# Kernel optimization log

Measured on AMD Instinct MI355X. Metric: run time of the kernel, lower is better.

Reference implementation:

```python
import jax, jax.numpy as jnp
import numpy as np

D_MODEL = 1024
D_K = 64
D_V = 64
TEMPERATURE = float(np.sqrt(D_K))
LN_EPS = 1e-5


def setup_inputs() -> dict:
    key = jax.random.key(0)
    ks = jax.random.split(key, 8)
    B, L = 8, 2048
    q = jax.random.normal(ks[0], (B, L, D_K), dtype=jnp.float32)
    k = jax.random.normal(ks[1], (B, L, D_K), dtype=jnp.float32)
    v = jax.random.normal(ks[2], (B, L, D_V), dtype=jnp.float32)
    residual = jax.random.normal(ks[3], (B, L, D_MODEL), dtype=jnp.float32)
    # fc: Linear(d_v, d_model), xavier-normal weight, zero-ish bias
    fc_w = jax.random.normal(ks[4], (D_MODEL, D_V), dtype=jnp.float32) * float(np.sqrt(2.0 / (D_V + D_MODEL)))
    fc_b = jnp.zeros((D_MODEL,), dtype=jnp.float32)
    ln_gamma = jnp.ones((D_MODEL,), dtype=jnp.float32)
    ln_beta = jnp.zeros((D_MODEL,), dtype=jnp.float32)
    return {"q": q, "k": k, "v": v, "residual": residual,
            "fc_w": fc_w, "fc_b": fc_b, "ln_gamma": ln_gamma, "ln_beta": ln_beta}


def reference(q, k, v, residual, fc_w, fc_b, ln_gamma, ln_beta):
    # scaled dot-product attention: scores [B, Lq, Lk]
    scores = jnp.einsum("bqd,bkd->bqk", q, k) / TEMPERATURE
    # module computes both log_softmax and softmax (shared logsumexp in a
    # fused kernel); log_attn is discarded by Attention.forward
    log_attn = jax.nn.log_softmax(scores, axis=2)
    attn = jnp.exp(log_attn)  # == softmax(scores); dropout is identity at eval
    out = jnp.einsum("bqk,bkv->bqv", attn, v)  # [B, Lq, d_v]
    # fc + residual + LayerNorm (dropout identity at eval)
    out = jnp.einsum("bqv,mv->bqm", out, fc_w) + fc_b
    x = out + residual
    mu = jnp.mean(x, axis=-1, keepdims=True)
    var = jnp.var(x, axis=-1, keepdims=True)
    return (x - mu) * jax.lax.rsqrt(var + LN_EPS) * ln_gamma + ln_beta
```

## Files before the change

### kernel.cpp

```cpp
#include <hip/hip_runtime.h>

typedef float  f32x4 __attribute__((ext_vector_type(4)));
typedef float  f4v   __attribute__((ext_vector_type(4)));
typedef short  s16x8 __attribute__((ext_vector_type(8)));
typedef unsigned short u16x4 __attribute__((ext_vector_type(4)));
typedef unsigned short u16;

#define DEVI static __device__ __forceinline__
#define AS1 __attribute__((address_space(1)))
#define AS3 __attribute__((address_space(3)))

DEVI u16 f2bf(float f) {
  unsigned int u = __builtin_bit_cast(unsigned int, f);
  u += 0x7FFFu + ((u >> 16) & 1u);
  return (u16)(u >> 16);
}

constexpr int B  = 8;
constexpr int L  = 2048;
constexpr int D  = 64;
constexpr int DM = 1024;

__global__ void prep_kernel(const float* __restrict__ k, const float* __restrict__ v,
                            const float* __restrict__ w,
                            u16* __restrict__ kbf, u16* __restrict__ vtbf,
                            u16* __restrict__ wbf) {
  __shared__ float tile[64 * 65];
  const int bid = blockIdx.x, tid = threadIdx.x;
  if (bid < 1024) {
    const int i = bid * 256 + tid;
    f4v f = ((const f4v*)k)[i];
    u16x4 o;
#pragma unroll
    for (int j = 0; j < 4; ++j) o[j] = f2bf(f[j] * 0.125f);
    ((u16x4*)kbf)[i] = o;
  } else if (bid < 1024 + 64) {
    const int i = (bid - 1024) * 256 + tid;
    f4v f = ((const f4v*)w)[i];
    u16x4 o;
#pragma unroll
    for (int j = 0; j < 4; ++j) o[j] = f2bf(f[j]);
    ((u16x4*)wbf)[i] = o;
  } else {
    const int t2 = bid - 1088;
    const int b = t2 >> 5, tt = t2 & 31;
    const float* vp = v + ((size_t)b * L + tt * 64) * D;
    for (int i = tid; i < 4096; i += 256) {
      const int r = i >> 6, c = i & 63;
      tile[c * 65 + r] = vp[i];
    }
    __syncthreads();
    u16* op = vtbf + (size_t)b * D * L + tt * 64;
    for (int i = tid; i < 4096; i += 256) {
      const int dv = i >> 6, kv = i & 63;
      op[(size_t)dv * L + kv] = f2bf(tile[dv * 65 + kv]);
    }
  }
}

__global__ __launch_bounds__(512) void attn_kernel(const float* __restrict__ q,
                                                   const u16* __restrict__ kbf,
                                                   const u16* __restrict__ vtbf,
                                                   float* __restrict__ Og) {
  const int blk = blockIdx.x;
  const int b = blk >> 5;
  const int qrow0 = (blk & 31) * 64;
  const int tid = threadIdx.x;
  const int wave = tid >> 6, lane = tid & 63;
  const int g = wave >> 1, h = wave & 1;
  const int lg = lane >> 4, ln = lane & 15;

  __shared__ __align__(16) u16   Kt[2][64 * 64];
  __shared__ __align__(16) u16   Vt[2][64 * 64];
  __shared__ __align__(16) u16   Pl[8][16 * 40];
  __shared__ float Macc[8][16][68];
  __shared__ float Lsum[8][16];

  s16x8 aq[2];
  {
    const float* qp = q + ((size_t)b * L + qrow0 + g * 16 + ln) * D + lg * 8;
#pragma unroll
    for (int kk = 0; kk < 2; ++kk) {
      f4v f0 = *(const f4v*)(qp + kk * 32);
      f4v f1 = *(const f4v*)(qp + kk * 32 + 4);
      s16x8 a;
#pragma unroll
      for (int j = 0; j < 4; ++j) { a[j] = (short)f2bf(f0[j]); a[4 + j] = (short)f2bf(f1[j]); }
      aq[kk] = a;
    }
  }

  const f32x4 zf = {0.f, 0.f, 0.f, 0.f};
  f32x4 acc[4];
#pragma unroll
  for (int i = 0; i < 4; ++i) acc[i] = zf;
  float lrow[4] = {0.f, 0.f, 0.f, 0.f};

  const u16* kb = kbf + (size_t)b * L * D;
  const u16* vb = vtbf + (size_t)b * D * L;

  auto stage = [&](int buf, int t) {
    const int kv0 = t * 64;
    const int row = tid >> 3, jl = tid & 7;
    const int js = jl ^ (row & 7);
    const u16* srcK = kb + (size_t)(kv0 + row) * D + js * 8;
    __builtin_amdgcn_global_load_lds(
        (const AS1 unsigned int*)srcK, (AS3 unsigned int*)&Kt[buf][tid * 8], 16, 0, 0);
    const u16* srcV = vb + (size_t)row * L + kv0 + js * 8;
    __builtin_amdgcn_global_load_lds(
        (const AS1 unsigned int*)srcV, (AS3 unsigned int*)&Vt[buf][tid * 8], 16, 0, 0);
  };

  stage(0, 0);

  for (int t = 0; t < 32; ++t) {
    __syncthreads();
    if (t + 1 < 32) stage((t + 1) & 1, t + 1);
    const int buf = t & 1;

    f32x4 s[2];
    s[0] = zf; s[1] = zf;
#pragma unroll
    for (int kk = 0; kk < 2; ++kk) {
#pragma unroll
      for (int fn2 = 0; fn2 < 2; ++fn2) {
        const int kvr = h * 32 + fn2 * 16 + ln;
        const int j = (kk * 4 + lg) ^ (kvr & 7);
        s16x8 bk = *(const s16x8*)&Kt[buf][kvr * 64 + j * 8];
        s[fn2] = __builtin_amdgcn_mfma_f32_16x16x32_bf16(aq[kk], bk, s[fn2], 0, 0, 0);
      }
    }

#pragma unroll
    for (int r = 0; r < 4; ++r) {
      const float p0 = __expf(s[0][r]);
      const float p1 = __expf(s[1][r]);
      lrow[r] += p0 + p1;
      Pl[wave][(lg * 4 + r) * 40 + ln]      = f2bf(p0);
      Pl[wave][(lg * 4 + r) * 40 + 16 + ln] = f2bf(p1);
    }

    asm volatile("" ::: "memory");

    s16x8 ap = *(const s16x8*)&Pl[wave][ln * 40 + lg * 8];
#pragma unroll
    for (int fn = 0; fn < 4; ++fn) {
      const int dv = fn * 16 + ln;
      const int j = (h * 4 + lg) ^ (dv & 7);
      s16x8 bv = *(const s16x8*)&Vt[buf][dv * 64 + j * 8];
      acc[fn] = __builtin_amdgcn_mfma_f32_16x16x32_bf16(ap, bv, acc[fn], 0, 0, 0);
    }
  }

#pragma unroll
  for (int r = 0; r < 4; ++r) {
#pragma unroll
    for (int off = 1; off < 16; off <<= 1) lrow[r] += __shfl_xor(lrow[r], off, 64);
    if (ln == 0) Lsum[wave][lg * 4 + r] = lrow[r];
  }
#pragma unroll
  for (int fn = 0; fn < 4; ++fn)
#pragma unroll
    for (int r = 0; r < 4; ++r)
      Macc[wave][lg * 4 + r][fn * 16 + ln] = acc[fn][r];
  __syncthreads();

  {
    const int row = tid >> 3, d0 = (tid & 7) * 8;
    const int g2 = row >> 4, r2 = row & 15;
    const float linv = 1.f / (Lsum[g2 * 2][r2] + Lsum[g2 * 2 + 1][r2]);
    f4v o0 = *(const f4v*)&Macc[g2 * 2][r2][d0]     + *(const f4v*)&Macc[g2 * 2 + 1][r2][d0];
    f4v o1 = *(const f4v*)&Macc[g2 * 2][r2][d0 + 4] + *(const f4v*)&Macc[g2 * 2 + 1][r2][d0 + 4];
#pragma unroll
    for (int j = 0; j < 4; ++j) { o0[j] *= linv; o1[j] *= linv; }
    float* dst = Og + ((size_t)b * L + qrow0 + row) * D + d0;
    *(f4v*)dst = o0;
    *(f4v*)(dst + 4) = o1;
  }
}

__global__ __launch_bounds__(512, 2) void fc_ln_kernel(const float* __restrict__ Og,
                                                       const u16* __restrict__ wbf,
                                                       const float* __restrict__ bias,
                                                       const float* __restrict__ resid,
                                                       const float* __restrict__ gamma,
                                                       const float* __restrict__ beta,
                                                       float* __restrict__ out) {
  __shared__ __align__(16) u16   Wl[1024 * 64];
  __shared__ __align__(16) float bl[1024];
  __shared__ __align__(16) float gl[1024];
  __shared__ __align__(16) float btl[1024];
  __shared__ float part[8][16][2];

  const int row0 = blockIdx.x * 32;
  const int tid = threadIdx.x;
  const int wave = tid >> 6, lane = tid & 63;
  const int rg = wave >> 2, mq = wave & 3;
  const int lg = lane >> 4, ln = lane & 15;
  const int row = row0 + rg * 16 + ln;
  const int m0 = mq * 256;

  f4v og0, og1, og2, og3;
  {
    const float* op = Og + (size_t)row * D + lg * 8;
    asm volatile("global_load_dwordx4 %0, %1, off"            : "=v"(og0) : "v"(op) : "memory");
    asm volatile("global_load_dwordx4 %0, %1, off offset:16"  : "=v"(og1) : "v"(op) : "memory");
    asm volatile("global_load_dwordx4 %0, %1, off offset:128" : "=v"(og2) : "v"(op) : "memory");
    asm volatile("global_load_dwordx4 %0, %1, off offset:144" : "=v"(og3) : "v"(op) : "memory");
  }
  f4v rsd[16];
  {
    const float* rp = resid + (size_t)row * DM + m0 + lg * 4;
#pragma unroll
    for (int fn = 0; fn < 16; ++fn)
      asm volatile("global_load_dwordx4 %0, %1, off offset:%c2"
                   : "=v"(rsd[fn]) : "v"(rp), "i"(fn * 64) : "memory");
  }

  {
#pragma unroll
    for (int i = 0; i < 16; ++i) {
      const int c = tid + i * 512;
      const int r = c >> 3, j = c & 7;
      const u16* src = wbf + r * 64 + (j ^ (r & 7)) * 8;
      __builtin_amdgcn_global_load_lds(
          (const AS1 unsigned int*)src, (AS3 unsigned int*)&Wl[c * 8], 16, 0, 0);
    }
    if (tid < 256) {
      __builtin_amdgcn_global_load_lds(
          (const AS1 unsigned int*)(bias + tid * 4), (AS3 unsigned int*)&bl[tid * 4], 16, 0, 0);
      __builtin_amdgcn_global_load_lds(
          (const AS1 unsigned int*)(beta + tid * 4), (AS3 unsigned int*)&btl[tid * 4], 16, 0, 0);
    } else {
      const int t2 = tid - 256;
      __builtin_amdgcn_global_load_lds(
          (const AS1 unsigned int*)(gamma + t2 * 4), (AS3 unsigned int*)&gl[t2 * 4], 16, 0, 0);
    }
  }

  __syncthreads();
  __builtin_amdgcn_sched_barrier(0);

  s16x8 bo[2];
  {
    f4v ogl[4] = {og0, og1, og2, og3};
#pragma unroll
    for (int kk = 0; kk < 2; ++kk) {
      s16x8 a;
#pragma unroll
      for (int j = 0; j < 4; ++j) {
        a[j]     = (short)f2bf(ogl[kk * 2][j]);
        a[4 + j] = (short)f2bf(ogl[kk * 2 + 1][j]);
      }
      bo[kk] = a;
    }
  }

  f32x4 acc[16];
  const int jb = ln & 7;
#pragma unroll
  for (int fn = 0; fn < 16; ++fn) {
    const int m = m0 + fn * 16 + ln;
    s16x8 aw0 = *(const s16x8*)&Wl[m * 64 + (lg ^ jb) * 8];
    s16x8 aw1 = *(const s16x8*)&Wl[m * 64 + ((4 + lg) ^ jb) * 8];
    acc[fn] = *(const f4v*)&bl[m0 + fn * 16 + lg * 4];
    acc[fn] = __builtin_amdgcn_mfma_f32_16x16x32_bf16(aw0, bo[0], acc[fn], 0, 0, 0);
    acc[fn] = __builtin_amdgcn_mfma_f32_16x16x32_bf16(aw1, bo[1], acc[fn], 0, 0, 0);
  }

  float sum = 0.f, ssq = 0.f;
#pragma unroll
  for (int fn = 0; fn < 16; ++fn) {
#pragma unroll
    for (int r = 0; r < 4; ++r) {
      const float x = acc[fn][r] + rsd[fn][r];
      acc[fn][r] = x;
      sum += x;
      ssq += x * x;
    }
  }
  sum += __shfl_xor(sum, 16, 64); ssq += __shfl_xor(ssq, 16, 64);
  sum += __shfl_xor(sum, 32, 64); ssq += __shfl_xor(ssq, 32, 64);
  if (lg == 0) { part[wave][ln][0] = sum; part[wave][ln][1] = ssq; }
  __syncthreads();
  float sm = 0.f, q2 = 0.f;
#pragma unroll
  for (int w2 = 0; w2 < 4; ++w2) {
    sm += part[rg * 4 + w2][ln][0];
    q2 += part[rg * 4 + w2][ln][1];
  }
  const float mu   = sm * (1.0f / 1024.0f);
  const float var  = q2 * (1.0f / 1024.0f) - mu * mu;
  const float rstd = rsqrtf(var + 1e-5f);

#pragma unroll
  for (int fn = 0; fn < 16; ++fn) {
    const int m4 = m0 + fn * 16 + lg * 4;
    const f4v gm = *(const f4v*)&gl[m4];
    const f4v bt = *(const f4v*)&btl[m4];
    f4v o;
#pragma unroll
    for (int r = 0; r < 4; ++r) o[r] = (acc[fn][r] - mu) * rstd * gm[r] + bt[r];
    *(f4v*)&out[(size_t)row * DM + m4] = o;
  }
}

extern "C" void kernel_launch(void* const* d_in, const int* in_sizes, int n_in,
                              void* d_out, int out_size, void* d_ws, size_t ws_size,
                              hipStream_t stream) {
  const float* q     = (const float*)d_in[0];
  const float* k     = (const float*)d_in[1];
  const float* v     = (const float*)d_in[2];
  const float* resid = (const float*)d_in[3];
  const float* fc_w  = (const float*)d_in[4];
  const float* fc_b  = (const float*)d_in[5];
  const float* gamma = (const float*)d_in[6];
  const float* beta  = (const float*)d_in[7];
  float* out = (float*)d_out;

  char* ws = (char*)d_ws;
  u16*   kbf  = (u16*)(ws);
  u16*   vtbf = (u16*)(ws + (2u << 20));
  u16*   wbf  = (u16*)(ws + (4u << 20));
  float* Og   = (float*)(ws + (4u << 20) + (128u << 10));

  prep_kernel<<<1344, 256, 0, stream>>>(k, v, fc_w, kbf, vtbf, wbf);
  attn_kernel<<<256, 512, 0, stream>>>(q, kbf, vtbf, Og);
  fc_ln_kernel<<<(B * L) / 32, 512, 0, stream>>>(Og, wbf, fc_b, resid, gamma, beta, out);
}
```

Measured before the change: 70.92 us.

## Process two row tiles per fc_ln block and prefetch the second tile's loads

```diff
diff --git a/kernel.cpp b/kernel.cpp
--- a/kernel.cpp
+++ b/kernel.cpp
@@ -192,30 +192,14 @@
   __shared__ __align__(16) float btl[1024];
   __shared__ float part[8][16][2];
 
-  const int row0 = blockIdx.x * 32;
   const int tid = threadIdx.x;
   const int wave = tid >> 6, lane = tid & 63;
   const int rg = wave >> 2, mq = wave & 3;
   const int lg = lane >> 4, ln = lane & 15;
-  const int row = row0 + rg * 16 + ln;
   const int m0 = mq * 256;
-
-  f4v og0, og1, og2, og3;
-  {
-    const float* op = Og + (size_t)row * D + lg * 8;
-    asm volatile("global_load_dwordx4 %0, %1, off"            : "=v"(og0) : "v"(op) : "memory");
-    asm volatile("global_load_dwordx4 %0, %1, off offset:16"  : "=v"(og1) : "v"(op) : "memory");
-    asm volatile("global_load_dwordx4 %0, %1, off offset:128" : "=v"(og2) : "v"(op) : "memory");
-    asm volatile("global_load_dwordx4 %0, %1, off offset:144" : "=v"(og3) : "v"(op) : "memory");
-  }
-  f4v rsd[16];
-  {
-    const float* rp = resid + (size_t)row * DM + m0 + lg * 4;
-#pragma unroll
-    for (int fn = 0; fn < 16; ++fn)
-      asm volatile("global_load_dwordx4 %0, %1, off offset:%c2"
-                   : "=v"(rsd[fn]) : "v"(rp), "i"(fn * 64) : "memory");
-  }
+  const int rowA = blockIdx.x * 64 + rg * 16 + ln;
+  const int rowB = rowA + 32;
+  const int jb = ln & 7;
 
   {
 #pragma unroll
@@ -238,70 +222,152 @@
     }
   }
 
-  __syncthreads();
+  f4v ogA0, ogA1, ogA2, ogA3;
+  {
+    const float* op = Og + (size_t)rowA * D + lg * 8;
+    asm volatile("global_load_dwordx4 %0, %1, off"            : "=v"(ogA0) : "v"(op) : "memory");
+    asm volatile("global_load_dwordx4 %0, %1, off offset:16"  : "=v"(ogA1) : "v"(op) : "memory");
+    asm volatile("global_load_dwordx4 %0, %1, off offset:128" : "=v"(ogA2) : "v"(op) : "memory");
+    asm volatile("global_load_dwordx4 %0, %1, off offset:144" : "=v"(ogA3) : "v"(op) : "memory");
+  }
+  f4v rsdA[16];
+  {
+    const float* rp = resid + (size_t)rowA * DM + m0 + lg * 4;
+#pragma unroll
+    for (int fn = 0; fn < 16; ++fn)
+      asm volatile("global_load_dwordx4 %0, %1, off offset:%c2"
+                   : "=v"(rsdA[fn]) : "v"(rp), "i"(fn * 64) : "memory");
+  }
+
+  asm volatile("s_waitcnt vmcnt(0)" ::: "memory");
   __builtin_amdgcn_sched_barrier(0);
-
-  s16x8 bo[2];
-  {
-    f4v ogl[4] = {og0, og1, og2, og3};
-#pragma unroll
-    for (int kk = 0; kk < 2; ++kk) {
+  __builtin_amdgcn_s_barrier();
+  __builtin_amdgcn_sched_barrier(0);
+
+  f32x4 acc[16];
+#pragma unroll
+  for (int fn = 0; fn < 16; ++fn)
+    acc[fn] = *(const f4v*)&bl[m0 + fn * 16 + lg * 4] + rsdA[fn];
+
+  f4v ogB0, ogB1, ogB2, ogB3;
+  {
+    const float* op = Og + (size_t)rowB * D + lg * 8;
+    asm volatile("global_load_dwordx4 %0, %1, off"            : "=v"(ogB0) : "v"(op) : "memory");
+    asm volatile("global_load_dwordx4 %0, %1, off offset:16"  : "=v"(ogB1) : "v"(op) : "memory");
+    asm volatile("global_load_dwordx4 %0, %1, off offset:128" : "=v"(ogB2) : "v"(op) : "memory");
+    asm volatile("global_load_dwordx4 %0, %1, off offset:144" : "=v"(ogB3) : "v"(op) : "memory");
+  }
+  f4v rsdB[16];
+  {
+    const float* rp = resid + (size_t)rowB * DM + m0 + lg * 4;
+#pragma unroll
+    for (int fn = 0; fn < 16; ++fn)
+      asm volatile("global_load_dwordx4 %0, %1, off offset:%c2"
+                   : "=v"(rsdB[fn]) : "v"(rp), "i"(fn * 64) : "memory");
+  }
+
+  {
+    s16x8 bo0, bo1;
+    {
       s16x8 a;
 #pragma unroll
-      for (int j = 0; j < 4; ++j) {
-        a[j]     = (short)f2bf(ogl[kk * 2][j]);
-        a[4 + j] = (short)f2bf(ogl[kk * 2 + 1][j]);
-      }
-      bo[kk] = a;
-    }
-  }
-
-  f32x4 acc[16];
-  const int jb = ln & 7;
-#pragma unroll
-  for (int fn = 0; fn < 16; ++fn) {
-    const int m = m0 + fn * 16 + ln;
-    s16x8 aw0 = *(const s16x8*)&Wl[m * 64 + (lg ^ jb) * 8];
-    s16x8 aw1 = *(const s16x8*)&Wl[m * 64 + ((4 + lg) ^ jb) * 8];
-    acc[fn] = *(const f4v*)&bl[m0 + fn * 16 + lg * 4];
-    acc[fn] = __builtin_amdgcn_mfma_f32_16x16x32_bf16(aw0, bo[0], acc[fn], 0, 0, 0);
-    acc[fn] = __builtin_amdgcn_mfma_f32_16x16x32_bf16(aw1, bo[1], acc[fn], 0, 0, 0);
-  }
-
-  float sum = 0.f, ssq = 0.f;
-#pragma unroll
-  for (int fn = 0; fn < 16; ++fn) {
-#pragma unroll
-    for (int r = 0; r < 4; ++r) {
-      const float x = acc[fn][r] + rsd[fn][r];
-      acc[fn][r] = x;
-      sum += x;
-      ssq += x * x;
-    }
-  }
-  sum += __shfl_xor(sum, 16, 64); ssq += __shfl_xor(ssq, 16, 64);
-  sum += __shfl_xor(sum, 32, 64); ssq += __shfl_xor(ssq, 32, 64);
-  if (lg == 0) { part[wave][ln][0] = sum; part[wave][ln][1] = ssq; }
-  __syncthreads();
-  float sm = 0.f, q2 = 0.f;
-#pragma unroll
-  for (int w2 = 0; w2 < 4; ++w2) {
-    sm += part[rg * 4 + w2][ln][0];
-    q2 += part[rg * 4 + w2][ln][1];
-  }
-  const float mu   = sm * (1.0f / 1024.0f);
-  const float var  = q2 * (1.0f / 1024.0f) - mu * mu;
-  const float rstd = rsqrtf(var + 1e-5f);
-
-#pragma unroll
-  for (int fn = 0; fn < 16; ++fn) {
-    const int m4 = m0 + fn * 16 + lg * 4;
-    const f4v gm = *(const f4v*)&gl[m4];
-    const f4v bt = *(const f4v*)&btl[m4];
-    f4v o;
-#pragma unroll
-    for (int r = 0; r < 4; ++r) o[r] = (acc[fn][r] - mu) * rstd * gm[r] + bt[r];
-    *(f4v*)&out[(size_t)row * DM + m4] = o;
+      for (int j = 0; j < 4; ++j) { a[j] = (short)f2bf(ogA0[j]); a[4 + j] = (short)f2bf(ogA1[j]); }
+      bo0 = a;
+#pragma unroll
+      for (int j = 0; j < 4; ++j) { a[j] = (short)f2bf(ogA2[j]); a[4 + j] = (short)f2bf(ogA3[j]); }
+      bo1 = a;
+    }
+#pragma unroll
+    for (int fn = 0; fn < 16; ++fn) {
+      const int m = m0 + fn * 16 + ln;
+      s16x8 aw0 = *(const s16x8*)&Wl[m * 64 + (lg ^ jb) * 8];
+      s16x8 aw1 = *(const s16x8*)&Wl[m * 64 + ((4 + lg) ^ jb) * 8];
+      acc[fn] = __builtin_amdgcn_mfma_f32_16x16x32_bf16(aw0, bo0, acc[fn], 0, 0, 0);
+      acc[fn] = __builtin_amdgcn_mfma_f32_16x16x32_bf16(aw1, bo1, acc[fn], 0, 0, 0);
+    }
+    float sum = 0.f, ssq = 0.f;
+#pragma unroll
+    for (int fn = 0; fn < 16; ++fn)
+#pragma unroll
+      for (int r = 0; r < 4; ++r) { const float x = acc[fn][r]; sum += x; ssq += x * x; }
+    sum += __shfl_xor(sum, 16, 64); ssq += __shfl_xor(ssq, 16, 64);
+    sum += __shfl_xor(sum, 32, 64); ssq += __shfl_xor(ssq, 32, 64);
+    if (lg == 0) { part[wave][ln][0] = sum; part[wave][ln][1] = ssq; }
+    asm volatile("s_waitcnt lgkmcnt(0)" ::: "memory");
+    __builtin_amdgcn_s_barrier();
+    __builtin_amdgcn_sched_barrier(0);
+    float sm = 0.f, q2 = 0.f;
+#pragma unroll
+    for (int w2 = 0; w2 < 4; ++w2) { sm += part[rg * 4 + w2][ln][0]; q2 += part[rg * 4 + w2][ln][1]; }
+    const float mu   = sm * (1.0f / 1024.0f);
+    const float var  = q2 * (1.0f / 1024.0f) - mu * mu;
+    const float rstd = rsqrtf(var + 1e-5f);
+#pragma unroll
+    for (int fn = 0; fn < 16; ++fn) {
+      const int m4 = m0 + fn * 16 + lg * 4;
+      const f4v gm = *(const f4v*)&gl[m4];
+      const f4v bt = *(const f4v*)&btl[m4];
+      f4v o;
+#pragma unroll
+      for (int r = 0; r < 4; ++r) o[r] = (acc[fn][r] - mu) * rstd * gm[r] + bt[r];
+      *(f4v*)&out[(size_t)rowA * DM + m4] = o;
+    }
+  }
+
+  asm volatile("s_waitcnt vmcnt(0)" ::: "memory");
+  __builtin_amdgcn_sched_barrier(0);
+  __builtin_amdgcn_s_barrier();
+  __builtin_amdgcn_sched_barrier(0);
+
+  {
+#pragma unroll
+    for (int fn = 0; fn < 16; ++fn)
+      acc[fn] = *(const f4v*)&bl[m0 + fn * 16 + lg * 4] + rsdB[fn];
+    s16x8 bo0, bo1;
+    {
+      s16x8 a;
+#pragma unroll
+      for (int j = 0; j < 4; ++j) { a[j] = (short)f2bf(ogB0[j]); a[4 + j] = (short)f2bf(ogB1[j]); }
+      bo0 = a;
+#pragma unroll
+      for (int j = 0; j < 4; ++j) { a[j] = (short)f2bf(ogB2[j]); a[4 + j] = (short)f2bf(ogB3[j]); }
+      bo1 = a;
+    }
+#pragma unroll
+    for (int fn = 0; fn < 16; ++fn) {
+      const int m = m0 + fn * 16 + ln;
+      s16x8 aw0 = *(const s16x8*)&Wl[m * 64 + (lg ^ jb) * 8];
+      s16x8 aw1 = *(const s16x8*)&Wl[m * 64 + ((4 + lg) ^ jb) * 8];
+      acc[fn] = __builtin_amdgcn_mfma_f32_16x16x32_bf16(aw0, bo0, acc[fn], 0, 0, 0);
+      acc[fn] = __builtin_amdgcn_mfma_f32_16x16x32_bf16(aw1, bo1, acc[fn], 0, 0, 0);
+    }
+    float sum = 0.f, ssq = 0.f;
+#pragma unroll
+    for (int fn = 0; fn < 16; ++fn)
+#pragma unroll
+      for (int r = 0; r < 4; ++r) { const float x = acc[fn][r]; sum += x; ssq += x * x; }
+    sum += __shfl_xor(sum, 16, 64); ssq += __shfl_xor(ssq, 16, 64);
+    sum += __shfl_xor(sum, 32, 64); ssq += __shfl_xor(ssq, 32, 64);
+    if (lg == 0) { part[wave][ln][0] = sum; part[wave][ln][1] = ssq; }
+    asm volatile("s_waitcnt lgkmcnt(0)" ::: "memory");
+    __builtin_amdgcn_s_barrier();
+    __builtin_amdgcn_sched_barrier(0);
+    float sm = 0.f, q2 = 0.f;
+#pragma unroll
+    for (int w2 = 0; w2 < 4; ++w2) { sm += part[rg * 4 + w2][ln][0]; q2 += part[rg * 4 + w2][ln][1]; }
+    const float mu   = sm * (1.0f / 1024.0f);
+    const float var  = q2 * (1.0f / 1024.0f) - mu * mu;
+    const float rstd = rsqrtf(var + 1e-5f);
+#pragma unroll
+    for (int fn = 0; fn < 16; ++fn) {
+      const int m4 = m0 + fn * 16 + lg * 4;
+      const f4v gm = *(const f4v*)&gl[m4];
+      const f4v bt = *(const f4v*)&btl[m4];
+      f4v o;
+#pragma unroll
+      for (int r = 0; r < 4; ++r) o[r] = (acc[fn][r] - mu) * rstd * gm[r] + bt[r];
+      *(f4v*)&out[(size_t)rowB * DM + m4] = o;
+    }
   }
 }
 
@@ -326,5 +392,5 @@
 
   prep_kernel<<<1344, 256, 0, stream>>>(k, v, fc_w, kbf, vtbf, wbf);
   attn_kernel<<<256, 512, 0, stream>>>(q, kbf, vtbf, Og);
-  fc_ln_kernel<<<(B * L) / 32, 512, 0, stream>>>(Og, wbf, fc_b, resid, gamma, beta, out);
-}
+  fc_ln_kernel<<<256, 512, 0, stream>>>(Og, wbf, fc_b, resid, gamma, beta, out);
+}
```

New measurement: 65.27 us. -8.0%, faster.
